# Kernel tuning notes

Measured on AMD Instinct MI355X. Metric: run time of the kernel, lower is better.

Reference implementation:

```python
import jax, jax.numpy as jnp
import numpy as np

B, S, E, H = 8, 512, 1024, 16
Dh = E // H
MAX_LEN = 512


def setup_inputs() -> dict:
    key = jax.random.key(0)
    ks = jax.random.split(key, 16)
    std = 1.0 / np.sqrt(E)
    inp = {
        "query": jax.random.normal(ks[0], (B, S, E), jnp.float32),
        "key": jax.random.normal(ks[1], (B, S, E), jnp.float32),
        "value": jax.random.normal(ks[2], (B, S, E), jnp.float32),
        "Wq": jax.random.normal(ks[3], (E, E), jnp.float32) * std,
        "bq": jax.random.normal(ks[4], (E,), jnp.float32) * std,
        "Wk": jax.random.normal(ks[5], (E, E), jnp.float32) * std,
        "bk": jax.random.normal(ks[6], (E,), jnp.float32) * std,
        "Wv": jax.random.normal(ks[7], (E, E), jnp.float32) * std,
        "bv": jax.random.normal(ks[8], (E,), jnp.float32) * std,
        "Wo": jax.random.normal(ks[9], (E, E), jnp.float32) * std,
        "bo": jax.random.normal(ks[10], (E,), jnp.float32) * std,
        "pos": jax.random.normal(ks[11], (MAX_LEN, 1, E), jnp.float32),
    }
    return inp


def reference(query, key, value, Wq, bq, Wk, bk, Wv, bv, Wo, bo, pos):
    b, sq, e = query.shape
    s = min(sq, key.shape[1])  # target_seq_length (static)
    scale = np.sqrt(Dh).astype(np.float32)
    pe = pos[:s, 0, :][None]  # [1, s, E] broadcast over batch
    q = query[:, :s] @ Wq.T + bq + pe
    k = key[:, :s] @ Wk.T + bk + pe
    v = value[:, :s] @ Wv.T + bv + pe
    # [b, s, H, Dh]
    q = q.reshape(b, s, H, Dh)
    k = k.reshape(b, s, H, Dh)
    v = v.reshape(b, s, H, Dh)
    scores = jnp.einsum("bqhd,bkhd->bhqk", q, k) / scale
    attn = jax.nn.softmax(scores, axis=-1)
    wv = jnp.einsum("bhqk,bkhd->bqhd", attn, v).reshape(b, s, e)
    return wv @ Wo.T + bo
```

## Files before the change

kernel.cpp:

```cpp
#include <hip/hip_runtime.h>
#include <hip/hip_bf16.h>

typedef __attribute__((ext_vector_type(8))) short bfx8;
typedef __attribute__((ext_vector_type(4))) short bfx4;
typedef __attribute__((ext_vector_type(4))) float fx4;

static __device__ __forceinline__ short f2bf(float f) {
  union { float f; unsigned u; } v; v.f = f;
  unsigned r = v.u + 0x7fffu + ((v.u >> 16) & 1u);
  return (short)(r >> 16);
}

static __device__ __forceinline__ void gld16(const void* g, void* l) {
  __builtin_amdgcn_global_load_lds(
      (const __attribute__((address_space(1))) void*)g,
      (__attribute__((address_space(3))) void*)l, 16, 0, 0);
}

constexpr int Bz = 8, Sq = 512, Em = 1024, Hn = 16, Dh = 64;
constexpr int Mrows = Bz * Sq;
constexpr size_t NE = (size_t)Mrows * Em;
constexpr size_t WE = (size_t)Em * Em;
constexpr int NT = Em / 64;

__global__ __launch_bounds__(256) void convert_kernel(
    const float* __restrict__ q, const float* __restrict__ k,
    const float* __restrict__ v,
    const float* __restrict__ Wq, const float* __restrict__ Wk,
    const float* __restrict__ Wv, const float* __restrict__ Wo,
    short* __restrict__ qx, short* __restrict__ kx, short* __restrict__ vx,
    short* __restrict__ wqb, short* __restrict__ wkb,
    short* __restrict__ wvb, short* __restrict__ wob)
{
  const size_t c = (size_t)blockIdx.x * 256 + threadIdx.x;
  constexpr size_t CI = NE / 8;
  constexpr size_t CW = WE / 8;
  const float* src; short* dst; size_t off;
  if (c < 3 * CI) {
    const int sgi = (int)(c / CI);
    src = sgi == 0 ? q : sgi == 1 ? k : v;
    dst = sgi == 0 ? qx : sgi == 1 ? kx : vx;
    off = (c - (size_t)sgi * CI) * 8;
  } else {
    const size_t w = c - 3 * CI;
    const int sgi = (int)(w / CW);
    src = sgi == 0 ? Wq : sgi == 1 ? Wk : sgi == 2 ? Wv : Wo;
    dst = sgi == 0 ? wqb : sgi == 1 ? wkb : sgi == 2 ? wvb : wob;
    off = (w - (size_t)sgi * CW) * 8;
  }
  fx4 a = *(const fx4*)(src + off);
  fx4 b = *(const fx4*)(src + off + 4);
  bfx8 o = { f2bf(a[0]), f2bf(a[1]), f2bf(a[2]), f2bf(a[3]),
             f2bf(b[0]), f2bf(b[1]), f2bf(b[2]), f2bf(b[3]) };
  *(bfx8*)(dst + off) = o;
}

__global__ __launch_bounds__(512, 2) void gemm_qkv_bf16(
    const short* __restrict__ qx, const short* __restrict__ kx,
    const short* __restrict__ vx,
    const short* __restrict__ Wqb, const short* __restrict__ Wkb,
    const short* __restrict__ Wvb,
    const float* __restrict__ bq, const float* __restrict__ bk,
    const float* __restrict__ bv,
    const float* __restrict__ pos,
    short* __restrict__ qb, short* __restrict__ kb, short* __restrict__ vb)
{
  __shared__ short SM[65536];

  const int z = blockIdx.z;
  const short* X = (z == 0) ? qx : (z == 1) ? kx : vx;
  const short* W = (z == 0) ? Wqb : (z == 1) ? Wkb : Wvb;
  const float* bias = (z == 0) ? bq : (z == 1) ? bk : bv;
  short* dst = (z == 0) ? qb : (z == 1) ? kb : vb;

  const int t0b = blockIdx.x * 256;
  const int f0 = blockIdx.y * 256;
  const int t = threadIdx.x, lane = t & 63, wave = t >> 6;
  const int wr = wave >> 2;
  const int wn = wave & 3;
  const int fr = lane & 15, fq = lane >> 4;

  const int srow = t >> 3;
  const int scc = (t & 7) ^ (srow & 7);
  const int sdst = wave * 512;

  const int sw0 = (fq ^ (fr & 7)) * 8;
  const int sw1 = ((4 + fq) ^ (fr & 7)) * 8;

  auto stageA = [&](int hh, int ktn, int pn) {
    const short* s = W + (size_t)(f0 + hh * 128 + srow) * Em + ktn * 64 + scc * 8;
    short* d = SM + pn * 32768 + hh * 8192 + sdst;
    gld16(s, d);
    gld16(s + (size_t)64 * Em, d + 4096);
  };
  auto stageB = [&](int hh, int ktn, int pn) {
    const short* s = X + (size_t)(t0b + hh * 128 + srow) * Em + ktn * 64 + scc * 8;
    short* d = SM + pn * 32768 + 16384 + hh * 8192 + sdst;
    gld16(s, d);
    gld16(s + (size_t)64 * Em, d + 4096);
  };

  fx4 acc[8][4] = {};

  stageA(0, 0, 0); stageA(1, 0, 0); stageB(0, 0, 0); stageB(1, 0, 0);
  __builtin_amdgcn_sched_barrier(0);
  asm volatile("s_waitcnt vmcnt(0)");
  __builtin_amdgcn_sched_barrier(0);
  __builtin_amdgcn_s_barrier();

  for (int kt = 0; kt < NT; ++kt) {
    const int p = kt & 1, pn = p ^ 1;
    const int ktn = (kt + 1 < NT) ? kt + 1 : 0;
    const short* Ab = SM + p * 32768 + wr * 8192;
    const short* Bb = SM + p * 32768 + 16384 + (wn >> 1) * 8192 + (wn & 1) * 4096;

    bfx8 bf[4][2];
#pragma unroll
    for (int q = 0; q < 4; ++q) {
      if (q == 0) {
#pragma unroll
        for (int cg = 0; cg < 4; ++cg) {
          bf[cg][0] = *(const bfx8*)&Bb[(cg * 16 + fr) * 64 + sw0];
          bf[cg][1] = *(const bfx8*)&Bb[(cg * 16 + fr) * 64 + sw1];
        }
      }
      bfx8 af[2][2];
#pragma unroll
      for (int rr2 = 0; rr2 < 2; ++rr2) {
        const int row = (q * 2 + rr2) * 16 + fr;
        af[rr2][0] = *(const bfx8*)&Ab[row * 64 + sw0];
        af[rr2][1] = *(const bfx8*)&Ab[row * 64 + sw1];
      }
      if (q == 0) { stageA(0, ktn, pn); stageA(1, ktn, pn); }
      if (q == 1) { stageB(0, ktn, pn); stageB(1, ktn, pn); }

      __builtin_amdgcn_sched_barrier(0);
      __builtin_amdgcn_s_barrier();
      __builtin_amdgcn_sched_barrier(0);

      __builtin_amdgcn_s_setprio(1);
#pragma unroll
      for (int rr2 = 0; rr2 < 2; ++rr2)
#pragma unroll
        for (int cg = 0; cg < 4; ++cg) {
          acc[q * 2 + rr2][cg] = __builtin_amdgcn_mfma_f32_16x16x32_bf16(
              af[rr2][0], bf[cg][0], acc[q * 2 + rr2][cg], 0, 0, 0);
          acc[q * 2 + rr2][cg] = __builtin_amdgcn_mfma_f32_16x16x32_bf16(
              af[rr2][1], bf[cg][1], acc[q * 2 + rr2][cg], 0, 0, 0);
        }
      __builtin_amdgcn_s_setprio(0);
      __builtin_amdgcn_sched_barrier(0);

      if (q == 3) {
        asm volatile("s_waitcnt vmcnt(0)");
        __builtin_amdgcn_sched_barrier(0);
      }
      __builtin_amdgcn_s_barrier();
    }
  }

  const int b = t0b >> 9;
  if (z < 2) {
#pragma unroll
    for (int fp = 0; fp < 2; ++fp) {
      if (fp) __syncthreads();
      if (wr == fp) {
#pragma unroll
        for (int rg = 0; rg < 8; ++rg) {
          const int nloc = rg * 16 + fq * 4;
          const int nng = f0 + fp * 128 + nloc;
          const fx4 bb = *(const fx4*)&bias[nng];
#pragma unroll
          for (int cg = 0; cg < 4; ++cg) {
            const int token = wn * 64 + cg * 16 + fr;
            const int s = (t0b + token) & (Sq - 1);
            const fx4 pe = *(const fx4*)&pos[(size_t)s * Em + nng];
            const fx4 a = acc[rg][cg];
            bfx4 o = { f2bf(a[0] + bb[0] + pe[0]), f2bf(a[1] + bb[1] + pe[1]),
                       f2bf(a[2] + bb[2] + pe[2]), f2bf(a[3] + bb[3] + pe[3]) };
            *(bfx4*)&SM[token * 136 + nloc] = o;
          }
        }
      }
      __syncthreads();
#pragma unroll
      for (int it = 0; it < 8; ++it) {
        const int flat = it * 512 + t;
        const int token = flat >> 4, ch = flat & 15;
        bfx8 val = *(const bfx8*)&SM[token * 136 + ch * 8];
        const int nng = f0 + fp * 128 + ch * 8;
        const int h = nng >> 6, d = nng & 63;
        const int s = (t0b + token) & (Sq - 1);
        *(bfx8*)&dst[(((size_t)b * Hn + h) * Sq + s) * Dh + d] = val;
      }
    }
  } else {
#pragma unroll
    for (int fp = 0; fp < 2; ++fp) {
      if (fp) __syncthreads();
      if (wr == fp) {
#pragma unroll
        for (int rg = 0; rg < 8; ++rg) {
          const int nloc = rg * 16 + fq * 4;
          const int nng = f0 + fp * 128 + nloc;
          const fx4 bb = *(const fx4*)&bias[nng];
#pragma unroll
          for (int cg = 0; cg < 4; ++cg) {
            const int token = wn * 64 + cg * 16 + fr;
            const int s = (t0b + token) & (Sq - 1);
            const fx4 pe = *(const fx4*)&pos[(size_t)s * Em + nng];
            const fx4 a = acc[rg][cg];
#pragma unroll
            for (int i = 0; i < 4; ++i)
              SM[(nloc + i) * 264 + token] = f2bf(a[i] + bb[i] + pe[i]);
          }
        }
      }
      __syncthreads();
      const int s0 = t0b & (Sq - 1);
#pragma unroll
      for (int it = 0; it < 8; ++it) {
        const int flat = it * 512 + t;
        const int row = flat >> 5, ch = flat & 31;
        bfx8 val = *(const bfx8*)&SM[row * 264 + ch * 8];
        const int nng = f0 + fp * 128 + row;
        const int h = nng >> 6, d = nng & 63;
        *(bfx8*)&dst[(((size_t)b * Hn + h) * Dh + d) * Sq + s0 + ch * 8] = val;
      }
    }
  }
}

constexpr int LDP = 136;

__global__ __launch_bounds__(256, 4) void gemm_out_bf16(
    const short* __restrict__ wv, const short* __restrict__ Wob,
    const float* __restrict__ bo, float* __restrict__ out)
{
  __shared__ short SMo[2 * 8192];
  short* As = SMo;
  short* Bs = SMo + 8192;

  const int m0 = blockIdx.x * 128;
  const int n0 = blockIdx.y * 128;
  const int t = threadIdx.x, lane = t & 63, wave = t >> 6;
  const int wr = wave >> 1, wc = wave & 1;
  const int fr = lane & 15, fq = lane >> 4;

  const int trow = t >> 3;
  const int scol = ((t & 7) ^ (trow & 7)) * 8;
  const short* gW = Wob + (size_t)(n0 + trow) * Em + scol;
  const short* gX = wv + (size_t)(m0 + trow) * Em + scol;
  short* lA = As + wave * 512;
  short* lB = Bs + wave * 512;

  const int sw0 = ((fq ^ (fr & 7)) * 8);
  const int sw1 = (((4 + fq) ^ (fr & 7)) * 8);

  fx4 acc[4][4] = {};

  for (int k0 = 0; k0 < Em; k0 += 64) {
#pragma unroll
    for (int r = 0; r < 4; ++r) {
      gld16(gW + (size_t)(32 * r) * Em + k0, lA + r * 2048);
      gld16(gX + (size_t)(32 * r) * Em + k0, lB + r * 2048);
    }
    __syncthreads();

#pragma unroll
    for (int ks = 0; ks < 2; ++ks) {
      const int sw = ks ? sw1 : sw0;
      bfx8 af[4], bf[4];
#pragma unroll
      for (int u = 0; u < 4; ++u)
        af[u] = *(const bfx8*)&As[(wr * 64 + u * 16 + fr) * 64 + sw];
#pragma unroll
      for (int v = 0; v < 4; ++v)
        bf[v] = *(const bfx8*)&Bs[(wc * 64 + v * 16 + fr) * 64 + sw];
#pragma unroll
      for (int u = 0; u < 4; ++u)
#pragma unroll
        for (int v = 0; v < 4; ++v)
          acc[u][v] = __builtin_amdgcn_mfma_f32_16x16x32_bf16(af[u], bf[v], acc[u][v], 0, 0, 0);
    }
    __syncthreads();
  }

#pragma unroll
  for (int u = 0; u < 4; ++u) {
    const int nn = n0 + wr * 64 + u * 16 + fq * 4;
    const fx4 bb = *(const fx4*)&bo[nn];
#pragma unroll
    for (int v = 0; v < 4; ++v) {
      const int m = m0 + wc * 64 + v * 16 + fr;
      fx4 val = acc[u][v];
      val[0] += bb[0]; val[1] += bb[1]; val[2] += bb[2]; val[3] += bb[3];
      *(fx4*)&out[(size_t)m * Em + nn] = val;
    }
  }
}

constexpr int KVB = 64, LDK = 72;

__global__ __launch_bounds__(256) void attn_kernel(
    const short* __restrict__ qb, const short* __restrict__ kb,
    const short* __restrict__ vb, short* __restrict__ wv)
{
  __shared__ short Ks[KVB * LDK];
  __shared__ short Vt[Dh * LDK];
  __shared__ short Ps[4][16 * LDK];

  const int bh = blockIdx.x;
  const int qt = blockIdx.y;
  const int t = threadIdx.x, lane = t & 63, wave = t >> 6;
  const int fr = lane & 15, fq = lane >> 4;

  const size_t base = (size_t)bh * Sq * Dh;
  const int q0 = qt * 64 + wave * 16;

  bfx8 qf[2];
  {
    const short* qp = qb + base + (size_t)(q0 + fr) * Dh;
    qf[0] = *(const bfx8*)(qp + fq * 8);
    qf[1] = *(const bfx8*)(qp + 32 + fq * 8);
  }

  const int kr = t >> 2, kc = (t & 3) * 16;
  const short* kbp = kb + base + (size_t)kr * Dh + kc;
  const short* vbp = vb + base + (size_t)kr * Sq + kc;

  {
    bfx8 k0 = *(const bfx8*)kbp;
    bfx8 k1 = *(const bfx8*)(kbp + 8);
    bfx8 v0 = *(const bfx8*)vbp;
    bfx8 v1 = *(const bfx8*)(vbp + 8);
    *(bfx8*)&Ks[kr * LDK + kc] = k0;
    *(bfx8*)&Ks[kr * LDK + kc + 8] = k1;
    *(bfx8*)&Vt[kr * LDK + kc] = v0;
    *(bfx8*)&Vt[kr * LDK + kc + 8] = v1;
  }
  __syncthreads();

  float mrow[4] = { -1e30f, -1e30f, -1e30f, -1e30f };
  float lrow[4] = { 0.f, 0.f, 0.f, 0.f };
  fx4 oacc[4] = {};

  for (int kv0 = 0; kv0 < Sq; kv0 += KVB) {
    const bool more = (kv0 + KVB) < Sq;
    bfx8 nk0, nk1, nv0, nv1;
    if (more) {
      const short* nk = kbp + (size_t)(kv0 + KVB) * Dh;
      const short* nv = vbp + (kv0 + KVB);
      nk0 = *(const bfx8*)nk;
      nk1 = *(const bfx8*)(nk + 8);
      nv0 = *(const bfx8*)nv;
      nv1 = *(const bfx8*)(nv + 8);
    }

    fx4 sa[4] = {};
#pragma unroll
    for (int nf = 0; nf < 4; ++nf) {
#pragma unroll
      for (int ks = 0; ks < 2; ++ks) {
        bfx8 kf = *(const bfx8*)&Ks[(nf * 16 + fr) * LDK + ks * 32 + fq * 8];
        sa[nf] = __builtin_amdgcn_mfma_f32_16x16x32_bf16(qf[ks], kf, sa[nf], 0, 0, 0);
      }
    }

#pragma unroll
    for (int i = 0; i < 4; ++i) {
      float mx = fmaxf(fmaxf(sa[0][i], sa[1][i]), fmaxf(sa[2][i], sa[3][i]));
      mx = fmaxf(mx, __shfl_xor(mx, 1));
      mx = fmaxf(mx, __shfl_xor(mx, 2));
      mx = fmaxf(mx, __shfl_xor(mx, 4));
      mx = fmaxf(mx, __shfl_xor(mx, 8));
      mx *= 0.125f;
      const float mn = fmaxf(mrow[i], mx);
      const float alpha = __expf(mrow[i] - mn);
      mrow[i] = mn;
      float rs = 0.f;
#pragma unroll
      for (int nf = 0; nf < 4; ++nf) {
        const float p = __expf(sa[nf][i] * 0.125f - mn);
        rs += p;
        Ps[wave][(fq * 4 + i) * LDK + nf * 16 + fr] = f2bf(p);
      }
      rs += __shfl_xor(rs, 1);
      rs += __shfl_xor(rs, 2);
      rs += __shfl_xor(rs, 4);
      rs += __shfl_xor(rs, 8);
      lrow[i] = lrow[i] * alpha + rs;
#pragma unroll
      for (int df = 0; df < 4; ++df) oacc[df][i] *= alpha;
    }

    bfx8 pf[2];
    pf[0] = *(const bfx8*)&Ps[wave][fr * LDK + fq * 8];
    pf[1] = *(const bfx8*)&Ps[wave][fr * LDK + 32 + fq * 8];
#pragma unroll
    for (int df = 0; df < 4; ++df) {
#pragma unroll
      for (int ks = 0; ks < 2; ++ks) {
        bfx8 vf = *(const bfx8*)&Vt[(df * 16 + fr) * LDK + ks * 32 + fq * 8];
        oacc[df] = __builtin_amdgcn_mfma_f32_16x16x32_bf16(pf[ks], vf, oacc[df], 0, 0, 0);
      }
    }
    __syncthreads();

    if (more) {
      *(bfx8*)&Ks[kr * LDK + kc] = nk0;
      *(bfx8*)&Ks[kr * LDK + kc + 8] = nk1;
      *(bfx8*)&Vt[kr * LDK + kc] = nv0;
      *(bfx8*)&Vt[kr * LDK + kc + 8] = nv1;
      __syncthreads();
    }
  }

  const int b = bh >> 4, h = bh & 15;
#pragma unroll
  for (int df = 0; df < 4; ++df) {
    const int d = df * 16 + fr;
#pragma unroll
    for (int i = 0; i < 4; ++i) {
      const int qrow = q0 + fq * 4 + i;
      const float o = oacc[df][i] / lrow[i];
      wv[((size_t)b * Sq + qrow) * Em + h * Dh + d] = f2bf(o);
    }
  }
}

extern "C" void kernel_launch(void* const* d_in, const int* in_sizes, int n_in,
                              void* d_out, int out_size, void* d_ws, size_t ws_size,
                              hipStream_t stream) {
  (void)in_sizes; (void)n_in; (void)out_size; (void)ws_size;
  const float* query = (const float*)d_in[0];
  const float* key   = (const float*)d_in[1];
  const float* value = (const float*)d_in[2];
  const float* Wq = (const float*)d_in[3];
  const float* bq = (const float*)d_in[4];
  const float* Wk = (const float*)d_in[5];
  const float* bk = (const float*)d_in[6];
  const float* Wv = (const float*)d_in[7];
  const float* bv = (const float*)d_in[8];
  const float* Wo = (const float*)d_in[9];
  const float* bo = (const float*)d_in[10];
  const float* pos = (const float*)d_in[11];

  short* qx = (short*)d_ws;
  short* kx = qx + NE;
  short* vx = kx + NE;
  short* Wqb = vx + NE;
  short* Wkb = Wqb + WE;
  short* Wvb = Wkb + WE;
  short* Wob = Wvb + WE;
  short* qb = Wob + WE;
  short* wv = qx;
  short* kb = (short*)d_out;
  short* vb = kb + NE;

  convert_kernel<<<dim3(8192), 256, 0, stream>>>(
      query, key, value, Wq, Wk, Wv, Wo, qx, kx, vx, Wqb, Wkb, Wvb, Wob);
  gemm_qkv_bf16<<<dim3(Mrows / 256, Em / 256, 3), 512, 0, stream>>>(
      qx, kx, vx, Wqb, Wkb, Wvb, bq, bk, bv, pos, qb, kb, vb);
  attn_kernel<<<dim3(Bz * Hn, Sq / 64), 256, 0, stream>>>(qb, kb, vb, wv);
  gemm_out_bf16<<<dim3(Mrows / 128, Em / 128), 256, 0, stream>>>(
      wv, Wob, bo, (float*)d_out);
}
```

Baseline: 111.0 us.

## Enlarge attention query tile, add lazy softmax rescale, skip final redundant prefetch

The attention kernel now runs 8 waves per block covering 128 query rows, so each K/V tile loaded into LDS is reused by twice as many queries and each thread loads half as much. The online softmax only rescales the accumulator when the running max grows by more than a threshold, which removes most exp and multiply work per tile. MFMA sections are raised in priority. The QKV GEMM also stops issuing the wasted prefetch and wait on its last k-iteration. Risks are halved grid size for attention and possible overflow or precision loss if scores grow within the lazy threshold.

```diff
diff --git a/kernel.cpp b/kernel.cpp
--- a/kernel.cpp
+++ b/kernel.cpp
@@ -110,7 +110,7 @@
 
   for (int kt = 0; kt < NT; ++kt) {
     const int p = kt & 1, pn = p ^ 1;
-    const int ktn = (kt + 1 < NT) ? kt + 1 : 0;
+    const bool pre = (kt + 1 < NT);
     const short* Ab = SM + p * 32768 + wr * 8192;
     const short* Bb = SM + p * 32768 + 16384 + (wn >> 1) * 8192 + (wn & 1) * 4096;
 
@@ -131,8 +131,8 @@
         af[rr2][0] = *(const bfx8*)&Ab[row * 64 + sw0];
         af[rr2][1] = *(const bfx8*)&Ab[row * 64 + sw1];
       }
-      if (q == 0) { stageA(0, ktn, pn); stageA(1, ktn, pn); }
-      if (q == 1) { stageB(0, ktn, pn); stageB(1, ktn, pn); }
+      if (q == 0 && pre) { stageA(0, kt + 1, pn); stageA(1, kt + 1, pn); }
+      if (q == 1 && pre) { stageB(0, kt + 1, pn); stageB(1, kt + 1, pn); }
 
       __builtin_amdgcn_sched_barrier(0);
       __builtin_amdgcn_s_barrier();
@@ -151,7 +151,7 @@
       __builtin_amdgcn_s_setprio(0);
       __builtin_amdgcn_sched_barrier(0);
 
-      if (q == 3) {
+      if (q == 3 && pre) {
         asm volatile("s_waitcnt vmcnt(0)");
         __builtin_amdgcn_sched_barrier(0);
       }
@@ -302,13 +302,13 @@
 
 constexpr int KVB = 64, LDK = 72;
 
-__global__ __launch_bounds__(256) void attn_kernel(
+__global__ __launch_bounds__(512) void attn_kernel(
     const short* __restrict__ qb, const short* __restrict__ kb,
     const short* __restrict__ vb, short* __restrict__ wv)
 {
   __shared__ short Ks[KVB * LDK];
   __shared__ short Vt[Dh * LDK];
-  __shared__ short Ps[4][16 * LDK];
+  __shared__ short Ps[8][16 * LDK];
 
   const int bh = blockIdx.x;
   const int qt = blockIdx.y;
@@ -316,7 +316,7 @@
   const int fr = lane & 15, fq = lane >> 4;
 
   const size_t base = (size_t)bh * Sq * Dh;
-  const int q0 = qt * 64 + wave * 16;
+  const int q0 = qt * 128 + wave * 16;
 
   bfx8 qf[2];
   {
@@ -325,19 +325,15 @@
     qf[1] = *(const bfx8*)(qp + 32 + fq * 8);
   }
 
-  const int kr = t >> 2, kc = (t & 3) * 16;
+  const int kr = t >> 3, kc = (t & 7) * 8;
   const short* kbp = kb + base + (size_t)kr * Dh + kc;
   const short* vbp = vb + base + (size_t)kr * Sq + kc;
 
   {
     bfx8 k0 = *(const bfx8*)kbp;
-    bfx8 k1 = *(const bfx8*)(kbp + 8);
     bfx8 v0 = *(const bfx8*)vbp;
-    bfx8 v1 = *(const bfx8*)(vbp + 8);
     *(bfx8*)&Ks[kr * LDK + kc] = k0;
-    *(bfx8*)&Ks[kr * LDK + kc + 8] = k1;
     *(bfx8*)&Vt[kr * LDK + kc] = v0;
-    *(bfx8*)&Vt[kr * LDK + kc + 8] = v1;
   }
   __syncthreads();
 
@@ -347,17 +343,14 @@
 
   for (int kv0 = 0; kv0 < Sq; kv0 += KVB) {
     const bool more = (kv0 + KVB) < Sq;
-    bfx8 nk0, nk1, nv0, nv1;
+    bfx8 nk0, nv0;
     if (more) {
-      const short* nk = kbp + (size_t)(kv0 + KVB) * Dh;
-      const short* nv = vbp + (kv0 + KVB);
-      nk0 = *(const bfx8*)nk;
-      nk1 = *(const bfx8*)(nk + 8);
-      nv0 = *(const bfx8*)nv;
-      nv1 = *(const bfx8*)(nv + 8);
+      nk0 = *(const bfx8*)(kbp + (size_t)(kv0 + KVB) * Dh);
+      nv0 = *(const bfx8*)(vbp + kv0 + KVB);
     }
 
     fx4 sa[4] = {};
+    __builtin_amdgcn_s_setprio(1);
 #pragma unroll
     for (int nf = 0; nf < 4; ++nf) {
 #pragma unroll
@@ -366,6 +359,7 @@
         sa[nf] = __builtin_amdgcn_mfma_f32_16x16x32_bf16(qf[ks], kf, sa[nf], 0, 0, 0);
       }
     }
+    __builtin_amdgcn_s_setprio(0);
 
 #pragma unroll
     for (int i = 0; i < 4; ++i) {
@@ -375,13 +369,17 @@
       mx = fmaxf(mx, __shfl_xor(mx, 4));
       mx = fmaxf(mx, __shfl_xor(mx, 8));
       mx *= 0.125f;
-      const float mn = fmaxf(mrow[i], mx);
-      const float alpha = __expf(mrow[i] - mn);
-      mrow[i] = mn;
+      if (mx > mrow[i] + 8.f) {
+        const float alpha = __expf(mrow[i] - mx);
+        mrow[i] = mx;
+        lrow[i] *= alpha;
+#pragma unroll
+        for (int df = 0; df < 4; ++df) oacc[df][i] *= alpha;
+      }
       float rs = 0.f;
 #pragma unroll
       for (int nf = 0; nf < 4; ++nf) {
-        const float p = __expf(sa[nf][i] * 0.125f - mn);
+        const float p = __expf(sa[nf][i] * 0.125f - mrow[i]);
         rs += p;
         Ps[wave][(fq * 4 + i) * LDK + nf * 16 + fr] = f2bf(p);
       }
@@ -389,14 +387,13 @@
       rs += __shfl_xor(rs, 2);
       rs += __shfl_xor(rs, 4);
       rs += __shfl_xor(rs, 8);
-      lrow[i] = lrow[i] * alpha + rs;
-#pragma unroll
-      for (int df = 0; df < 4; ++df) oacc[df][i] *= alpha;
+      lrow[i] += rs;
     }
 
     bfx8 pf[2];
     pf[0] = *(const bfx8*)&Ps[wave][fr * LDK + fq * 8];
     pf[1] = *(const bfx8*)&Ps[wave][fr * LDK + 32 + fq * 8];
+    __builtin_amdgcn_s_setprio(1);
 #pragma unroll
     for (int df = 0; df < 4; ++df) {
 #pragma unroll
@@ -405,13 +402,12 @@
         oacc[df] = __builtin_amdgcn_mfma_f32_16x16x32_bf16(pf[ks], vf, oacc[df], 0, 0, 0);
       }
     }
+    __builtin_amdgcn_s_setprio(0);
     __syncthreads();
 
     if (more) {
       *(bfx8*)&Ks[kr * LDK + kc] = nk0;
-      *(bfx8*)&Ks[kr * LDK + kc + 8] = nk1;
       *(bfx8*)&Vt[kr * LDK + kc] = nv0;
-      *(bfx8*)&Vt[kr * LDK + kc + 8] = nv1;
       __syncthreads();
     }
   }
@@ -462,7 +458,7 @@
       query, key, value, Wq, Wk, Wv, Wo, qx, kx, vx, Wqb, Wkb, Wvb, Wob);
   gemm_qkv_bf16<<<dim3(Mrows / 256, Em / 256, 3), 512, 0, stream>>>(
       qx, kx, vx, Wqb, Wkb, Wvb, bq, bk, bv, pos, qb, kb, vb);
-  attn_kernel<<<dim3(Bz * Hn, Sq / 64), 256, 0, stream>>>(qb, kb, vb, wv);
+  attn_kernel<<<dim3(Bz * Hn, Sq / 128), 512, 0, stream>>>(qb, kb, vb, wv);
   gemm_out_bf16<<<dim3(Mrows / 128, Em / 128), 256, 0, stream>>>(
       wv, Wob, bo, (float*)d_out);
 }
```

New measurement: 109.7 us. About the same (-1.2%).
